# Kernel optimization log

Hardware: AMD Instinct MI355X
Metric: run time of the kernel (lower is better)

Reference implementation:

```python
import jax, jax.numpy as jnp
import numpy as np

N = 10000      # nodes
DIN = 1024     # input feature dim
H = 256        # hidden dim
NC = 3         # classes
EDGE_P = 0.002 # ~avg degree 20


def _lin(key, fin, fout):
    s = 1.0 / np.sqrt(fin)
    kw, kb = jax.random.split(key)
    W = jax.random.uniform(kw, (fin, fout), jnp.float32, -s, s)
    b = jax.random.uniform(kb, (fout,), jnp.float32, -s, s)
    return W, b


def setup_inputs() -> dict:
    key = jax.random.key(0)
    ks = jax.random.split(key, 10)
    features = jax.random.normal(ks[0], (N, DIN), jnp.float32)
    # sparse weighted adjacency with zero diagonal (dense storage, as the module expects)
    mask = jax.random.uniform(ks[1], (N, N)) < EDGE_P
    wts = jax.random.uniform(ks[2], (N, N), jnp.float32)
    adj = jnp.where(mask, wts, 0.0) * (1.0 - jnp.eye(N, dtype=jnp.float32))
    W0, b0 = _lin(ks[3], DIN, H)
    W1, b1 = _lin(ks[4], H, H)
    W2, b2 = _lin(ks[5], H, H)
    C1w, c1b = _lin(ks[6], 2 * H, H)
    C2w, c2b = _lin(ks[7], H, H // 2)
    C3w, c3b = _lin(ks[8], H // 2, NC)
    return {"features": features, "adj": adj,
            "W0": W0, "b0": b0, "W1": W1, "b1": b1, "W2": W2, "b2": b2,
            "C1w": C1w, "c1b": c1b, "C2w": C2w, "c2b": c2b, "C3w": C3w, "c3b": c3b}


def _gcn_norm(adj):
    # PyG GCNConv: add self-loops (weight 1), symmetric deg^{-1/2} normalization.
    A = adj + jnp.eye(adj.shape[0], dtype=adj.dtype)
    deg = A.sum(axis=1)
    dinv = jnp.where(deg > 0, jax.lax.rsqrt(deg), 0.0)
    return dinv[:, None] * A * dinv[None, :]


def reference(features, adj, W0, b0, W1, b1, W2, b2, C1w, c1b, C2w, c2b, C3w, c3b):
    An = _gcn_norm(adj)                       # [N, N] normalized adjacency
    x = features
    for W, b in ((W0, b0), (W1, b1), (W2, b2)):
        x = jax.nn.relu(An @ (x @ W) + b)     # linear -> aggregate -> bias -> relu
        # dropout is identity in eval mode
    g = jnp.concatenate([x.max(axis=0), x.mean(axis=0)])  # [2H]
    h = jax.nn.relu(g @ C1w + c1b)
    h = jax.nn.relu(h @ C2w + c2b)
    return h @ C3w + c3b                      # [NC] logits
```

## Files before the change

### kernel.cpp

```cpp
#include <hip/hip_runtime.h>
#include <hip/hip_bf16.h>

#define NN 10000
#define FDIN 1024
#define HH 256
#define CAP 64
#define MPAD 10112

typedef unsigned short u16;
typedef unsigned int u32;
typedef __attribute__((ext_vector_type(8))) short short8;
typedef __attribute__((ext_vector_type(4))) float f32x4;

__device__ __forceinline__ float ld_in(const void* p, size_t i, int bf) {
    if (bf) {
        unsigned short u = ((const unsigned short*)p)[i];
        return __uint_as_float(((unsigned int)u) << 16);
    }
    return ((const float*)p)[i];
}

__device__ __forceinline__ u16 bf16bits(float x) {
    __hip_bfloat16 h = __float2bfloat16(x);
    return *(u16*)&h;
}

__device__ __forceinline__ float bf16val(u16 u) {
    return __uint_as_float(((unsigned int)u) << 16);
}

__global__ __launch_bounds__(256) void k_detect(const u16* __restrict__ feat, int* flag) {
    __shared__ int s;
    if (threadIdx.x == 0) s = 0;
    __syncthreads();
    u16 u = feat[2 * threadIdx.x];
    int e = (u >> 7) & 0xFF;
    if (e >= 100 && e <= 137) atomicAdd(&s, 1);
    __syncthreads();
    if (threadIdx.x == 0) *flag = (s >= 128) ? 1 : 0;
}

__global__ __launch_bounds__(256) void k_scan(const void* __restrict__ adj,
                                              const int* __restrict__ flag,
                                              int* __restrict__ ellc,
                                              float* __restrict__ ellv,
                                              int* __restrict__ cnt,
                                              float* __restrict__ dinv) {
    int i = blockIdx.x;
    int tid = threadIdx.x;
    __shared__ int s_cnt;
    __shared__ float s_sum;
    if (tid == 0) { s_cnt = 0; s_sum = 0.f; }
    __syncthreads();
    int bf = *flag;
    float lsum = 0.f;
    if (bf) {
        const uint4* p = (const uint4*)((const unsigned short*)adj + (size_t)i * NN);
        for (int t = tid; t < NN / 8; t += 256) {
            uint4 q = p[t];
            unsigned int w_[4] = {q.x, q.y, q.z, q.w};
            #pragma unroll
            for (int w = 0; w < 4; ++w) {
                #pragma unroll
                for (int hh = 0; hh < 2; ++hh) {
                    unsigned short u = (unsigned short)(w_[w] >> (16 * hh));
                    if (u) {
                        float v = bf16val(u);
                        lsum += v;
                        int slot = atomicAdd(&s_cnt, 1);
                        if (slot < CAP) {
                            ellc[(size_t)i * CAP + slot] = t * 8 + w * 2 + hh;
                            ellv[(size_t)i * CAP + slot] = v;
                        }
                    }
                }
            }
        }
    } else {
        const float4* p = (const float4*)((const float*)adj + (size_t)i * NN);
        for (int t = tid; t < NN / 4; t += 256) {
            float4 q = p[t];
            float v_[4] = {q.x, q.y, q.z, q.w};
            #pragma unroll
            for (int w = 0; w < 4; ++w) {
                float v = v_[w];
                if (v != 0.f) {
                    lsum += v;
                    int slot = atomicAdd(&s_cnt, 1);
                    if (slot < CAP) {
                        ellc[(size_t)i * CAP + slot] = t * 4 + w;
                        ellv[(size_t)i * CAP + slot] = v;
                    }
                }
            }
        }
    }
    for (int off = 32; off > 0; off >>= 1) lsum += __shfl_down(lsum, off, 64);
    if ((tid & 63) == 0) atomicAdd(&s_sum, lsum);
    __syncthreads();
    if (tid == 0) {
        float deg = s_sum + 1.0f;
        dinv[i] = rsqrtf(deg);
        cnt[i] = s_cnt < CAP ? s_cnt : CAP;
    }
}

#define FEAT_BLOCKS (MPAD * FDIN / 8 / 256)

__global__ __launch_bounds__(256) void k_conv(const void* __restrict__ feat,
                                              const void* __restrict__ W0,
                                              const void* __restrict__ W1,
                                              const void* __restrict__ W2,
                                              const int* __restrict__ flag,
                                              u16* __restrict__ featb,
                                              u16* __restrict__ w0t,
                                              u16* __restrict__ w1t,
                                              u16* __restrict__ w2t) {
    int f = *flag;
    int bid = blockIdx.x;
    if (bid < FEAT_BLOCKS) {
        int idx = bid * 256 + threadIdx.x;
        int row = idx >> 7;
        int c0 = (idx & 127) * 8;
        u16 outv[8];
        if (row < NN) {
            if (f) {
                uint4 v = *(const uint4*)((const u16*)feat + (size_t)row * FDIN + c0);
                *(uint4*)(featb + (size_t)row * FDIN + c0) = v;
                return;
            }
            const float* fp = (const float*)feat + (size_t)row * FDIN + c0;
            float4 v0 = *(const float4*)fp;
            float4 v1 = *(const float4*)(fp + 4);
            float vv[8] = {v0.x, v0.y, v0.z, v0.w, v1.x, v1.y, v1.z, v1.w};
            #pragma unroll
            for (int e = 0; e < 8; ++e) outv[e] = bf16bits(vv[e]);
        } else {
            #pragma unroll
            for (int e = 0; e < 8; ++e) outv[e] = 0;
        }
        *(uint4*)(featb + (size_t)row * FDIN + c0) = *(const uint4*)outv;
        return;
    }
    int idx = (bid - FEAT_BLOCKS) * 256 + threadIdx.x;
    const void* W; u16* Wt; int K;
    if (idx < FDIN * HH)                { W = W0; Wt = w0t; K = FDIN; }
    else if (idx < FDIN * HH + HH * HH) { W = W1; Wt = w1t; K = HH; idx -= FDIN * HH; }
    else                                { W = W2; Wt = w2t; K = HH; idx -= FDIN * HH + HH * HH; }
    int k = idx >> 8, n = idx & 255;
    Wt[(size_t)n * K + k] = bf16bits(ld_in(W, (size_t)idx, f));
}


__device__ __forceinline__ void g_load(const u16* A, const u16* Bt, int K, int m0, int n0,
                                       int tid, int k0, uint4* sa, uint4* sb) {
    #pragma unroll
    for (int q = 0; q < 2; ++q) {
        int c = q * 256 + tid, row = c >> 3, b = (c & 7) << 4;
        sa[q] = *(const uint4*)((const unsigned char*)(A + (size_t)(m0 + row) * K + k0) + b);
    }
    #pragma unroll
    for (int q = 0; q < 4; ++q) {
        int c = q * 256 + tid, n = c >> 3, b = (c & 7) << 4;
        sb[q] = *(const uint4*)((const unsigned char*)(Bt + (size_t)(n0 + n) * K + k0) + b);
    }
}

__device__ __forceinline__ void lds_store(unsigned char* Asb, unsigned char* Bsb, int tid,
                                          const uint4* sa, const uint4* sb) {
    #pragma unroll
    for (int q = 0; q < 2; ++q) {
        int c = q * 256 + tid, row = c >> 3, b = (c & 7) << 4;
        *(uint4*)(Asb + row * 128 + (b ^ ((row & 7) << 4))) = sa[q];
    }
    #pragma unroll
    for (int q = 0; q < 4; ++q) {
        int c = q * 256 + tid, n = c >> 3, b = (c & 7) << 4;
        *(uint4*)(Bsb + n * 128 + (b ^ ((n & 7) << 4))) = sb[q];
    }
}

__device__ __forceinline__ void compute64(const unsigned char* Asb, const unsigned char* Bsb,
                                          int l, int wm, int wn, f32x4 acc[2][4]) {
    #pragma unroll
    for (int kk = 0; kk < 2; ++kk) {
        int kb = kk * 64 + ((l >> 4) << 4);
        short8 av[2], bv[4];
        #pragma unroll
        for (int i = 0; i < 2; ++i) {
            int row = wm * 32 + i * 16 + (l & 15);
            av[i] = *(const short8*)(Asb + row * 128 + (kb ^ ((row & 7) << 4)));
        }
        #pragma unroll
        for (int j = 0; j < 4; ++j) {
            int n = wn * 64 + j * 16 + (l & 15);
            bv[j] = *(const short8*)(Bsb + n * 128 + (kb ^ ((n & 7) << 4)));
        }
        #pragma unroll
        for (int i = 0; i < 2; ++i)
            #pragma unroll
            for (int j = 0; j < 4; ++j)
                acc[i][j] = __builtin_amdgcn_mfma_f32_16x16x32_bf16(av[i], bv[j], acc[i][j], 0, 0, 0);
    }
}

__global__ __launch_bounds__(256) void k_mfma(const u16* __restrict__ A,
                                              const u16* __restrict__ Bt,
                                              u16* __restrict__ Y, int K) {
    __shared__ uint4 As4[512];
    __shared__ uint4 Bs4[1024];
    unsigned char* Asb = (unsigned char*)As4;
    unsigned char* Bsb = (unsigned char*)Bs4;
    const int tid = threadIdx.x;
    const int l = tid & 63;
    const int wid = tid >> 6;
    const int wm = wid >> 1, wn = wid & 1;
    const int m0 = blockIdx.y * 64;
    const int n0 = blockIdx.x * 128;

    f32x4 acc[2][4] = {};
    uint4 sa[2], sb[4], ta[2], tb[4];
    g_load(A, Bt, K, m0, n0, tid, 0, sa, sb);
    const int nt = K >> 6;
    for (int t = 0; t < nt; t += 2) {
        __syncthreads();
        lds_store(Asb, Bsb, tid, sa, sb);
        __syncthreads();
        g_load(A, Bt, K, m0, n0, tid, (t + 1) << 6, ta, tb);
        compute64(Asb, Bsb, l, wm, wn, acc);
        __syncthreads();
        lds_store(Asb, Bsb, tid, ta, tb);
        __syncthreads();
        if (t + 2 < nt) g_load(A, Bt, K, m0, n0, tid, (t + 2) << 6, sa, sb);
        compute64(Asb, Bsb, l, wm, wn, acc);
    }
    #pragma unroll
    for (int i = 0; i < 2; ++i) {
        int r0 = m0 + wm * 32 + i * 16 + ((l >> 4) << 2);
        #pragma unroll
        for (int j = 0; j < 4; ++j) {
            int col = n0 + wn * 64 + j * 16 + (l & 15);
            #pragma unroll
            for (int r = 0; r < 4; ++r)
                Y[(size_t)(r0 + r) * HH + col] = bf16bits(acc[i][j][r]);
        }
    }
}

__global__ __launch_bounds__(128) void k_agg(const u32* __restrict__ y,
                                             const int* __restrict__ ellc,
                                             const float* __restrict__ ellv,
                                             const int* __restrict__ cnt,
                                             const float* __restrict__ dinv,
                                             const void* __restrict__ bias,
                                             const int* __restrict__ flag,
                                             u32* __restrict__ xout) {
    int i = blockIdx.x, j = threadIdx.x;
    int f = *flag;
    float di = dinv[i];
    u32 w = y[(size_t)i * 128 + j];
    float a0 = di * bf16val((u16)(w & 0xffff));
    float a1 = di * bf16val((u16)(w >> 16));
    int c_ = cnt[i];
    for (int e = 0; e < c_; ++e) {
        int c = ellc[(size_t)i * CAP + e];
        float s = ellv[(size_t)i * CAP + e] * dinv[c];
        u32 v = y[(size_t)c * 128 + j];
        a0 = fmaf(s, bf16val((u16)(v & 0xffff)), a0);
        a1 = fmaf(s, bf16val((u16)(v >> 16)), a1);
    }
    float v0 = fmaf(di, a0, ld_in(bias, (size_t)(2 * j), f));
    float v1 = fmaf(di, a1, ld_in(bias, (size_t)(2 * j + 1), f));
    v0 = v0 > 0.f ? v0 : 0.f;
    v1 = v1 > 0.f ? v1 : 0.f;
    xout[(size_t)i * 128 + j] = (u32)bf16bits(v0) | ((u32)bf16bits(v1) << 16);
}

__global__ __launch_bounds__(256) void k_pool(const u16* __restrict__ x,
                                              float* __restrict__ pmax,
                                              float* __restrict__ psum) {
    int j = threadIdx.x, b = blockIdx.x;
    int r0 = b * 250;
    float m = 0.f, s = 0.f;
    for (int r = r0; r < r0 + 250; ++r) {
        float v = bf16val(x[(size_t)r * HH + j]);
        m = fmaxf(m, v);
        s += v;
    }
    pmax[b * HH + j] = m;
    psum[b * HH + j] = s;
}

__global__ __launch_bounds__(256) void k_head(const float* __restrict__ pmax,
                                              const float* __restrict__ psum,
                                              const void* C1w, const void* c1b,
                                              const void* C2w, const void* c2b,
                                              const void* C3w, const void* c3b,
                                              const int* __restrict__ flag,
                                              void* __restrict__ out) {
    __shared__ float gs[2 * HH], h1[HH], h2[HH / 2];
    int j = threadIdx.x;
    int f = *flag;
    float m = 0.f, s = 0.f;
    #pragma unroll 4
    for (int b = 0; b < 40; ++b) {
        m = fmaxf(m, pmax[b * HH + j]);
        s += psum[b * HH + j];
    }
    gs[j] = m;
    gs[HH + j] = s * (1.0f / (float)NN);
    __syncthreads();
    float a = 0.f;
    for (int k = 0; k < 2 * HH; ++k) a = fmaf(gs[k], ld_in(C1w, (size_t)k * HH + j, f), a);
    a += ld_in(c1b, j, f);
    h1[j] = a > 0.f ? a : 0.f;
    __syncthreads();
    if (j < HH / 2) {
        float b2_ = 0.f;
        for (int k = 0; k < HH; ++k) b2_ = fmaf(h1[k], ld_in(C2w, (size_t)k * (HH / 2) + j, f), b2_);
        b2_ += ld_in(c2b, j, f);
        h2[j] = b2_ > 0.f ? b2_ : 0.f;
    }
    __syncthreads();
    if (j < 3) {
        float o = 0.f;
        for (int k = 0; k < HH / 2; ++k) o = fmaf(h2[k], ld_in(C3w, (size_t)k * 3 + j, f), o);
        o += ld_in(c3b, j, f);
        if (f) ((__hip_bfloat16*)out)[j] = __float2bfloat16(o);
        else   ((float*)out)[j] = o;
    }
}

extern "C" void kernel_launch(void* const* d_in, const int* in_sizes, int n_in,
                              void* d_out, int out_size, void* d_ws, size_t ws_size,
                              hipStream_t stream) {
    const void* feat = d_in[0];
    const void* adj  = d_in[1];
    const void* W0 = d_in[2];  const void* b0 = d_in[3];
    const void* W1 = d_in[4];  const void* b1 = d_in[5];
    const void* W2 = d_in[6];  const void* b2 = d_in[7];
    const void* C1w = d_in[8]; const void* c1b = d_in[9];
    const void* C2w = d_in[10]; const void* c2b = d_in[11];
    const void* C3w = d_in[12]; const void* c3b = d_in[13];

    char* ws = (char*)d_ws;
    size_t o = 0;
    auto take = [&](size_t bytes) -> void* {
        void* p = ws + o;
        o += (bytes + 255) & ~(size_t)255;
        return p;
    };
    int*   flag  = (int*)take(4);
    float* dinv  = (float*)take((size_t)NN * 4);
    int*   cnt   = (int*)take((size_t)NN * 4);
    int*   ellc  = (int*)take((size_t)NN * CAP * 4);
    float* ellv  = (float*)take((size_t)NN * CAP * 4);
    u16*   featb = (u16*)take((size_t)MPAD * FDIN * 2);
    u16*   w0t   = (u16*)take((size_t)HH * FDIN * 2);
    u16*   w1t   = (u16*)take((size_t)HH * HH * 2);
    u16*   w2t   = (u16*)take((size_t)HH * HH * 2);
    u16*   xbuf  = (u16*)take((size_t)MPAD * HH * 2);
    u16*   ybuf  = (u16*)take((size_t)MPAD * HH * 2);
    float* pmax  = (float*)take((size_t)40 * HH * 4);
    float* psum  = (float*)take((size_t)40 * HH * 4);

    k_detect<<<1, 256, 0, stream>>>((const u16*)feat, flag);
    k_scan<<<NN, 256, 0, stream>>>(adj, flag, ellc, ellv, cnt, dinv);
    int conv_blocks = FEAT_BLOCKS + (FDIN * HH + 2 * HH * HH) / 256;
    k_conv<<<conv_blocks, 256, 0, stream>>>(feat, W0, W1, W2, flag, featb, w0t, w1t, w2t);

    dim3 gg(2, MPAD / 64);
    k_mfma<<<gg, 256, 0, stream>>>(featb, w0t, ybuf, FDIN);
    k_agg<<<NN, 128, 0, stream>>>((const u32*)ybuf, ellc, ellv, cnt, dinv, b0, flag, (u32*)xbuf);
    k_mfma<<<gg, 256, 0, stream>>>(xbuf, w1t, ybuf, HH);
    k_agg<<<NN, 128, 0, stream>>>((const u32*)ybuf, ellc, ellv, cnt, dinv, b1, flag, (u32*)xbuf);
    k_mfma<<<gg, 256, 0, stream>>>(xbuf, w2t, ybuf, HH);
    k_agg<<<NN, 128, 0, stream>>>((const u32*)ybuf, ellc, ellv, cnt, dinv, b2, flag, (u32*)xbuf);

    k_pool<<<40, 256, 0, stream>>>(xbuf, pmax, psum);
    k_head<<<1, 256, 0, stream>>>(pmax, psum, C1w, c1b, C2w, c2b, C3w, c3b, flag, d_out);
}
```

Measured before the change: 417.2 us.

## Fuse dtype detect, adjacency scan and conversions into one kernel; skip feature copy

Merges the dtype-detection, adjacency-to-ELL scan and weight/feature conversion kernels into a single launch. Each block recomputes the dtype flag locally with a ballot instead of waiting on a separate kernel. The scan now skips all-zero 16-byte chunks before per-element checks. For bf16 inputs the first GEMM reads features directly instead of copying them, with row masking replacing the padded buffer. This removes launches and a large copy, at the cost of redundant flag computation per block and a bounds check in the GEMM load.

```diff
diff --git a/kernel.cpp b/kernel.cpp
--- a/kernel.cpp
+++ b/kernel.cpp
@@ -6,6 +6,8 @@
 #define HH 256
 #define CAP 64
 #define MPAD 10112
+#define WT_BLOCKS 1536
+#define FCONV_BLOCKS 5000
 
 typedef unsigned short u16;
 typedef unsigned int u32;
@@ -29,126 +31,117 @@
     return __uint_as_float(((unsigned int)u) << 16);
 }
 
-__global__ __launch_bounds__(256) void k_detect(const u16* __restrict__ feat, int* flag) {
-    __shared__ int s;
-    if (threadIdx.x == 0) s = 0;
+__device__ __forceinline__ int local_flag(const void* feat, int tid, int* cnts) {
+    u16 u = ((const u16*)feat)[2 * tid];
+    int e = (u >> 7) & 0xFF;
+    bool pred = (e >= 100 && e <= 137);
+    unsigned long long b = __ballot(pred);
+    if ((tid & 63) == 0) cnts[tid >> 6] = __popcll(b);
     __syncthreads();
-    u16 u = feat[2 * threadIdx.x];
-    int e = (u >> 7) & 0xFF;
-    if (e >= 100 && e <= 137) atomicAdd(&s, 1);
-    __syncthreads();
-    if (threadIdx.x == 0) *flag = (s >= 128) ? 1 : 0;
-}
-
-__global__ __launch_bounds__(256) void k_scan(const void* __restrict__ adj,
-                                              const int* __restrict__ flag,
-                                              int* __restrict__ ellc,
-                                              float* __restrict__ ellv,
-                                              int* __restrict__ cnt,
-                                              float* __restrict__ dinv) {
-    int i = blockIdx.x;
-    int tid = threadIdx.x;
+    return (cnts[0] + cnts[1] + cnts[2] + cnts[3]) >= 128;
+}
+
+__global__ __launch_bounds__(256) void k_scanconv(const void* __restrict__ feat,
+                                                  const void* __restrict__ adj,
+                                                  const void* __restrict__ W0,
+                                                  const void* __restrict__ W1,
+                                                  const void* __restrict__ W2,
+                                                  int* __restrict__ flag,
+                                                  int* __restrict__ ellc,
+                                                  float* __restrict__ ellv,
+                                                  int* __restrict__ cnt,
+                                                  float* __restrict__ dinv,
+                                                  u16* __restrict__ featb,
+                                                  u16* __restrict__ w0t,
+                                                  u16* __restrict__ w1t,
+                                                  u16* __restrict__ w2t) {
+    __shared__ int cnts[4];
     __shared__ int s_cnt;
     __shared__ float s_sum;
+    int tid = threadIdx.x;
+    int bid = blockIdx.x;
     if (tid == 0) { s_cnt = 0; s_sum = 0.f; }
-    __syncthreads();
-    int bf = *flag;
-    float lsum = 0.f;
-    if (bf) {
-        const uint4* p = (const uint4*)((const unsigned short*)adj + (size_t)i * NN);
-        for (int t = tid; t < NN / 8; t += 256) {
-            uint4 q = p[t];
-            unsigned int w_[4] = {q.x, q.y, q.z, q.w};
-            #pragma unroll
-            for (int w = 0; w < 4; ++w) {
+    int f = local_flag(feat, tid, cnts);
+    if (bid == 0 && tid == 0) *flag = f;
+
+    if (bid < NN) {
+        int i = bid;
+        float lsum = 0.f;
+        if (f) {
+            const uint4* p = (const uint4*)((const u16*)adj + (size_t)i * NN);
+            for (int t = tid; t < NN / 8; t += 256) {
+                uint4 q = p[t];
+                if ((q.x | q.y | q.z | q.w) == 0u) continue;
+                unsigned int w_[4] = {q.x, q.y, q.z, q.w};
                 #pragma unroll
-                for (int hh = 0; hh < 2; ++hh) {
-                    unsigned short u = (unsigned short)(w_[w] >> (16 * hh));
-                    if (u) {
-                        float v = bf16val(u);
+                for (int w = 0; w < 4; ++w) {
+                    #pragma unroll
+                    for (int hh = 0; hh < 2; ++hh) {
+                        unsigned short u = (unsigned short)(w_[w] >> (16 * hh));
+                        if (u) {
+                            float v = bf16val(u);
+                            lsum += v;
+                            int slot = atomicAdd(&s_cnt, 1);
+                            if (slot < CAP) {
+                                ellc[(size_t)i * CAP + slot] = t * 8 + w * 2 + hh;
+                                ellv[(size_t)i * CAP + slot] = v;
+                            }
+                        }
+                    }
+                }
+            }
+        } else {
+            const uint4* p = (const uint4*)((const float*)adj + (size_t)i * NN);
+            for (int t = tid; t < NN / 4; t += 256) {
+                uint4 qi = p[t];
+                if ((qi.x | qi.y | qi.z | qi.w) == 0u) continue;
+                unsigned int w_[4] = {qi.x, qi.y, qi.z, qi.w};
+                #pragma unroll
+                for (int w = 0; w < 4; ++w) {
+                    float v = __uint_as_float(w_[w]);
+                    if (v != 0.f) {
                         lsum += v;
                         int slot = atomicAdd(&s_cnt, 1);
                         if (slot < CAP) {
-                            ellc[(size_t)i * CAP + slot] = t * 8 + w * 2 + hh;
+                            ellc[(size_t)i * CAP + slot] = t * 4 + w;
                             ellv[(size_t)i * CAP + slot] = v;
                         }
                     }
                 }
             }
         }
-    } else {
-        const float4* p = (const float4*)((const float*)adj + (size_t)i * NN);
-        for (int t = tid; t < NN / 4; t += 256) {
-            float4 q = p[t];
-            float v_[4] = {q.x, q.y, q.z, q.w};
-            #pragma unroll
-            for (int w = 0; w < 4; ++w) {
-                float v = v_[w];
-                if (v != 0.f) {
-                    lsum += v;
-                    int slot = atomicAdd(&s_cnt, 1);
-                    if (slot < CAP) {
-                        ellc[(size_t)i * CAP + slot] = t * 4 + w;
-                        ellv[(size_t)i * CAP + slot] = v;
-                    }
-                }
-            }
-        }
-    }
-    for (int off = 32; off > 0; off >>= 1) lsum += __shfl_down(lsum, off, 64);
-    if ((tid & 63) == 0) atomicAdd(&s_sum, lsum);
-    __syncthreads();
-    if (tid == 0) {
-        float deg = s_sum + 1.0f;
-        dinv[i] = rsqrtf(deg);
-        cnt[i] = s_cnt < CAP ? s_cnt : CAP;
-    }
-}
-
-#define FEAT_BLOCKS (MPAD * FDIN / 8 / 256)
-
-__global__ __launch_bounds__(256) void k_conv(const void* __restrict__ feat,
-                                              const void* __restrict__ W0,
-                                              const void* __restrict__ W1,
-                                              const void* __restrict__ W2,
-                                              const int* __restrict__ flag,
-                                              u16* __restrict__ featb,
-                                              u16* __restrict__ w0t,
-                                              u16* __restrict__ w1t,
-                                              u16* __restrict__ w2t) {
-    int f = *flag;
-    int bid = blockIdx.x;
-    if (bid < FEAT_BLOCKS) {
-        int idx = bid * 256 + threadIdx.x;
-        int row = idx >> 7;
-        int c0 = (idx & 127) * 8;
-        u16 outv[8];
-        if (row < NN) {
-            if (f) {
-                uint4 v = *(const uint4*)((const u16*)feat + (size_t)row * FDIN + c0);
-                *(uint4*)(featb + (size_t)row * FDIN + c0) = v;
-                return;
-            }
-            const float* fp = (const float*)feat + (size_t)row * FDIN + c0;
-            float4 v0 = *(const float4*)fp;
-            float4 v1 = *(const float4*)(fp + 4);
-            float vv[8] = {v0.x, v0.y, v0.z, v0.w, v1.x, v1.y, v1.z, v1.w};
-            #pragma unroll
-            for (int e = 0; e < 8; ++e) outv[e] = bf16bits(vv[e]);
-        } else {
-            #pragma unroll
-            for (int e = 0; e < 8; ++e) outv[e] = 0;
-        }
-        *(uint4*)(featb + (size_t)row * FDIN + c0) = *(const uint4*)outv;
+        for (int off = 32; off > 0; off >>= 1) lsum += __shfl_down(lsum, off, 64);
+        if ((tid & 63) == 0) atomicAdd(&s_sum, lsum);
+        __syncthreads();
+        if (tid == 0) {
+            float deg = s_sum + 1.0f;
+            dinv[i] = rsqrtf(deg);
+            cnt[i] = s_cnt < CAP ? s_cnt : CAP;
+        }
         return;
     }
-    int idx = (bid - FEAT_BLOCKS) * 256 + threadIdx.x;
-    const void* W; u16* Wt; int K;
-    if (idx < FDIN * HH)                { W = W0; Wt = w0t; K = FDIN; }
-    else if (idx < FDIN * HH + HH * HH) { W = W1; Wt = w1t; K = HH; idx -= FDIN * HH; }
-    else                                { W = W2; Wt = w2t; K = HH; idx -= FDIN * HH + HH * HH; }
-    int k = idx >> 8, n = idx & 255;
-    Wt[(size_t)n * K + k] = bf16bits(ld_in(W, (size_t)idx, f));
+    if (bid < NN + WT_BLOCKS) {
+        int idx = (bid - NN) * 256 + tid;
+        const void* W; u16* Wt; int K;
+        if (idx < FDIN * HH)                { W = W0; Wt = w0t; K = FDIN; }
+        else if (idx < FDIN * HH + HH * HH) { W = W1; Wt = w1t; K = HH; idx -= FDIN * HH; }
+        else                                { W = W2; Wt = w2t; K = HH; idx -= FDIN * HH + HH * HH; }
+        int k = idx >> 8, n = idx & 255;
+        Wt[(size_t)n * K + k] = bf16bits(ld_in(W, (size_t)idx, f));
+        return;
+    }
+    if (f) return;
+    int idx = (bid - NN - WT_BLOCKS) * 256 + tid;
+    int row = idx >> 7;
+    int c0 = (idx & 127) * 8;
+    const float* fp = (const float*)feat + (size_t)row * FDIN + c0;
+    float4 v0 = *(const float4*)fp;
+    float4 v1 = *(const float4*)(fp + 4);
+    float vv[8] = {v0.x, v0.y, v0.z, v0.w, v1.x, v1.y, v1.z, v1.w};
+    u16 outv[8];
+    #pragma unroll
+    for (int e = 0; e < 8; ++e) outv[e] = bf16bits(vv[e]);
+    *(uint4*)(featb + (size_t)row * FDIN + c0) = *(const uint4*)outv;
 }
 
 
@@ -157,7 +150,10 @@
     #pragma unroll
     for (int q = 0; q < 2; ++q) {
         int c = q * 256 + tid, row = c >> 3, b = (c & 7) << 4;
-        sa[q] = *(const uint4*)((const unsigned char*)(A + (size_t)(m0 + row) * K + k0) + b);
+        uint4 v = {0u, 0u, 0u, 0u};
+        if (m0 + row < NN)
+            v = *(const uint4*)((const unsigned char*)(A + (size_t)(m0 + row) * K + k0) + b);
+        sa[q] = v;
     }
     #pragma unroll
     for (int q = 0; q < 4; ++q) {
@@ -204,13 +200,16 @@
     }
 }
 
-__global__ __launch_bounds__(256) void k_mfma(const u16* __restrict__ A,
+__global__ __launch_bounds__(256) void k_mfma(const u16* __restrict__ A1,
+                                              const u16* __restrict__ A2,
                                               const u16* __restrict__ Bt,
+                                              const int* __restrict__ flag,
                                               u16* __restrict__ Y, int K) {
     __shared__ uint4 As4[512];
     __shared__ uint4 Bs4[1024];
     unsigned char* Asb = (unsigned char*)As4;
     unsigned char* Bsb = (unsigned char*)Bs4;
+    const u16* A = (*flag) ? A1 : A2;
     const int tid = threadIdx.x;
     const int l = tid & 63;
     const int wid = tid >> 6;
@@ -355,7 +354,7 @@
     int*   cnt   = (int*)take((size_t)NN * 4);
     int*   ellc  = (int*)take((size_t)NN * CAP * 4);
     float* ellv  = (float*)take((size_t)NN * CAP * 4);
-    u16*   featb = (u16*)take((size_t)MPAD * FDIN * 2);
+    u16*   featb = (u16*)take((size_t)NN * FDIN * 2);
     u16*   w0t   = (u16*)take((size_t)HH * FDIN * 2);
     u16*   w1t   = (u16*)take((size_t)HH * HH * 2);
     u16*   w2t   = (u16*)take((size_t)HH * HH * 2);
@@ -364,17 +363,15 @@
     float* pmax  = (float*)take((size_t)40 * HH * 4);
     float* psum  = (float*)take((size_t)40 * HH * 4);
 
-    k_detect<<<1, 256, 0, stream>>>((const u16*)feat, flag);
-    k_scan<<<NN, 256, 0, stream>>>(adj, flag, ellc, ellv, cnt, dinv);
-    int conv_blocks = FEAT_BLOCKS + (FDIN * HH + 2 * HH * HH) / 256;
-    k_conv<<<conv_blocks, 256, 0, stream>>>(feat, W0, W1, W2, flag, featb, w0t, w1t, w2t);
+    k_scanconv<<<NN + WT_BLOCKS + FCONV_BLOCKS, 256, 0, stream>>>(
+        feat, adj, W0, W1, W2, flag, ellc, ellv, cnt, dinv, featb, w0t, w1t, w2t);
 
     dim3 gg(2, MPAD / 64);
-    k_mfma<<<gg, 256, 0, stream>>>(featb, w0t, ybuf, FDIN);
+    k_mfma<<<gg, 256, 0, stream>>>((const u16*)feat, featb, w0t, flag, ybuf, FDIN);
     k_agg<<<NN, 128, 0, stream>>>((const u32*)ybuf, ellc, ellv, cnt, dinv, b0, flag, (u32*)xbuf);
-    k_mfma<<<gg, 256, 0, stream>>>(xbuf, w1t, ybuf, HH);
+    k_mfma<<<gg, 256, 0, stream>>>(xbuf, xbuf, w1t, flag, ybuf, HH);
     k_agg<<<NN, 128, 0, stream>>>((const u32*)ybuf, ellc, ellv, cnt, dinv, b1, flag, (u32*)xbuf);
-    k_mfma<<<gg, 256, 0, stream>>>(xbuf, w2t, ybuf, HH);
+    k_mfma<<<gg, 256, 0, stream>>>(xbuf, xbuf, w2t, flag, ybuf, HH);
     k_agg<<<NN, 128, 0, stream>>>((const u32*)ybuf, ellc, ellv, cnt, dinv, b2, flag, (u32*)xbuf);
 
     k_pool<<<40, 256, 0, stream>>>(xbuf, pmax, psum);
```

Measured after the change: 385.8 us. -7.5%, faster.
